# Performance work log

Measured on AMD Instinct MI355X. Metric: run time of the kernel, lower is better.

Reference implementation:

```python
import jax, jax.numpy as jnp
import numpy as np

B, N, DIM, H, DH, P = 4, 4096, 256, 8, 64, 2
INNER = H * DH  # 512


def setup_inputs() -> dict:
    key = jax.random.key(0)
    ks = jax.random.split(key, 10)
    w = lambda k, shape: jax.random.normal(k, shape, dtype=jnp.float32) * 0.02
    return dict(
        x=jax.random.normal(ks[0], (B, N, DIM), dtype=jnp.float32),
        prev_x=jax.random.normal(ks[1], (B, N, DIM), dtype=jnp.float32),
        ln_q_g=jnp.ones((2 * DIM,), jnp.float32), ln_q_b=jnp.zeros((2 * DIM,), jnp.float32),
        ln_k_g=jnp.ones((DIM,), jnp.float32), ln_k_b=jnp.zeros((DIM,), jnp.float32),
        ln_v_g=jnp.ones((DIM,), jnp.float32), ln_v_b=jnp.zeros((DIM,), jnp.float32),
        Wq=w(ks[2], (2 * DIM, INNER)),            # to_q, bias=False
        Wk=w(ks[3], (DIM, INNER)), bk=jnp.zeros((INNER,), jnp.float32),
        Wv=w(ks[4], (DIM, INNER)), bv=jnp.zeros((INNER,), jnp.float32),
        Woff=w(ks[5], (H * P, INNER)),            # 1x1 conv == linear over channels
        boff=jax.random.uniform(ks[6], (H * P,), jnp.float32, -1.0, 1.0),
        Wout=w(ks[7], (DIM, INNER)), bout=jnp.zeros((DIM,), jnp.float32),
    )


def _ln(x, g, b):
    m = x.mean(-1, keepdims=True)
    v = ((x - m) ** 2).mean(-1, keepdims=True)
    return (x - m) * jax.lax.rsqrt(v + 1e-5) * g + b


def reference(x, prev_x, ln_q_g, ln_q_b, ln_k_g, ln_k_b, ln_v_g, ln_v_b,
              Wq, Wk, bk, Wv, bv, Woff, boff, Wout, bout):
    scale = DH ** -0.5
    # queries from cat(x, prev_x) along feature dim
    q = _ln(jnp.concatenate([x, prev_x], axis=-1), ln_q_g, ln_q_b) @ Wq  # (B,N,INNER)
    # learned per-head, per-point offsets (1x1 conv over channels)
    offsets = (q @ Woff.T + boff).reshape(B, N, H, P).transpose(0, 2, 3, 1)  # (B,H,P,N)
    # K/V from cat(x, prev_x) along batch dim -> KV length 2N per (b,h)
    kv = jnp.concatenate([x, prev_x], axis=0)  # (2B,N,DIM)
    k = (_ln(kv, ln_k_g, ln_k_b) @ Wk + bk).reshape(2, B, N, H, DH).transpose(1, 3, 4, 0, 2).reshape(B, H, DH, 2 * N)
    v = (_ln(kv, ln_v_g, ln_v_b) @ Wv + bv).reshape(2, B, N, H, DH).transpose(1, 3, 4, 0, 2).reshape(B, H, DH, 2 * N)
    # sampling positions: pos + offset, clamped, truncated to int (matches torch .long())
    pos = jnp.arange(N, dtype=jnp.float32)
    samp = jnp.clip(pos[None, None, None, :] + offsets, 0, 2 * N - 1).astype(jnp.int32)  # (B,H,P,N)
    idx = samp.transpose(0, 1, 3, 2)[:, :, None, :, :]  # (B,H,1,N,P)
    k_s = jnp.take_along_axis(k[:, :, :, None, :], idx, axis=-1)  # (B,H,DH,N,P)
    v_s = jnp.take_along_axis(v[:, :, :, None, :], idx, axis=-1)  # (B,H,DH,N,P)
    qh = q.reshape(B, N, H, DH).transpose(0, 2, 1, 3) * scale     # (B,H,N,DH)
    sim = jnp.einsum('bhnd,bhdnp->bhnp', qh, k_s)                  # (B,H,N,P)
    attn = jax.nn.softmax(sim, axis=-1)
    out = jnp.einsum('bhnp,bhdnp->bhnd', attn, v_s)                # (B,H,N,DH)
    out = out.transpose(0, 2, 1, 3).reshape(B, N, INNER) @ Wout.T + bout  # (B,N,DIM)
    return out, offsets
```

## Files before the change

### kernel.cpp

```cpp
#include <hip/hip_runtime.h>
#include <hip/hip_bf16.h>
#include <math.h>

#define B_    4
#define N_    4096
#define DIM_  256
#define H_    8
#define DH_   64
#define P_    2
#define INNER_ 512
#define BN_   (B_ * N_)
#define KVR_  (2 * BN_)

typedef short v8s  __attribute__((ext_vector_type(8)));
typedef short v4s  __attribute__((ext_vector_type(4)));
typedef float v4f  __attribute__((ext_vector_type(4)));

__device__ __forceinline__ short f2b(float x) {
    __hip_bfloat16 h = __float2bfloat16(x);
    return *reinterpret_cast<short*>(&h);
}
__device__ __forceinline__ float b2f(short s) {
    __hip_bfloat16 h = *reinterpret_cast<__hip_bfloat16*>(&s);
    return __bfloat162float(h);
}

__device__ __forceinline__ void async16(const void* g, void* l) {
    __builtin_amdgcn_global_load_lds(
        (const __attribute__((address_space(1))) void*)g,
        (__attribute__((address_space(3))) void*)l, 16, 0, 0);
}

__device__ __forceinline__ void storeRow(float* p, float4 f0, float4 f1, float4 f2, float4 f3) {
    ((float4*)p)[0] = f0; ((float4*)p)[1] = f1; ((float4*)p)[2] = f2; ((float4*)p)[3] = f3;
}
__device__ __forceinline__ void storeRow(__hip_bfloat16* p, float4 f0, float4 f1, float4 f2, float4 f3) {
    v8s o0, o1;
    o0[0]=f2b(f0.x); o0[1]=f2b(f0.y); o0[2]=f2b(f0.z); o0[3]=f2b(f0.w);
    o0[4]=f2b(f1.x); o0[5]=f2b(f1.y); o0[6]=f2b(f1.z); o0[7]=f2b(f1.w);
    o1[0]=f2b(f2.x); o1[1]=f2b(f2.y); o1[2]=f2b(f2.z); o1[3]=f2b(f2.w);
    o1[4]=f2b(f3.x); o1[5]=f2b(f3.y); o1[6]=f2b(f3.z); o1[7]=f2b(f3.w);
    ((v8s*)p)[0] = o0; ((v8s*)p)[1] = o1;
}

__global__ __launch_bounds__(256) void prep_all(
    const float* __restrict__ Wq, const float* __restrict__ gq, const float* __restrict__ betaq,
    const float* __restrict__ Wk, const float* __restrict__ gk, const float* __restrict__ betak,
    const float* __restrict__ bk,
    const float* __restrict__ Wv, const float* __restrict__ gv, const float* __restrict__ betav,
    const float* __restrict__ bv,
    const float* __restrict__ Woff, const float* __restrict__ Wout,
    short* __restrict__ Wq2t, float* __restrict__ bq2,
    short* __restrict__ Wkvt, float* __restrict__ bkv,
    float* __restrict__ Wcomb, float* __restrict__ braw, short* __restrict__ Woutb) {
    __shared__ float sm[272];
    const int bid = blockIdx.x, t = threadIdx.x;

    if (bid < 1536) {
        const float *W, *g, *beta, *bias_in;
        short* Wt; float* b2; int K, n; float scale;
        if (bid < 512)       { W=Wq; g=gq; beta=betaq; bias_in=nullptr; Wt=Wq2t; b2=bq2; K=512; n=bid;        scale=0.125f; }
        else if (bid < 1024) { W=Wk; g=gk; beta=betak; bias_in=bk; Wt=Wkvt;           b2=bkv;       K=256; n=bid-512;  scale=1.f; }
        else                 { W=Wv; g=gv; beta=betav; bias_in=bv; Wt=Wkvt+512*256;   b2=bkv+512;   K=256; n=bid-1024; scale=1.f; }
        float partial = 0.f;
        for (int k = t; k < K; k += 256) {
            float w = W[k * 512 + n];
            Wt[(size_t)n * K + k] = f2b(scale * g[k] * w);
            partial += beta[k] * w;
        }
        sm[t] = partial;
        __syncthreads();
        for (int s = 128; s > 0; s >>= 1) {
            if (t < s) sm[t] += sm[t + s];
            __syncthreads();
        }
        if (t == 0) b2[n] = scale * ((bias_in ? bias_in[n] : 0.f) + sm[0]);
    } else if (bid < 2048) {
        const int k = bid - 1536;
        const int hp = t & 15, jg = t >> 4;
        float p = 0.f;
        for (int j = jg; j < INNER_; j += 16)
            p += Wq[k * INNER_ + j] * Woff[hp * INNER_ + j];
        sm[jg * 17 + hp] = p;
        __syncthreads();
        if (t < 16) {
            float s = 0.f;
            for (int i = 0; i < 16; i++) s += sm[i * 17 + t];
            Wcomb[k * 16 + t] = gq[k] * s;
            braw[k * 16 + t]  = betaq[k] * s;
        }
    } else {
        const int i0 = (bid - 2048) * 1024 + t * 4;
        float4 f = *(const float4*)(Wout + i0);
        v4s o;
        o[0] = f2b(f.x); o[1] = f2b(f.y); o[2] = f2b(f.z); o[3] = f2b(f.w);
        *(v4s*)(Woutb + i0) = o;
    }
}

__global__ void bcomb_sum(const float* __restrict__ braw, const float* __restrict__ boff,
                          float* __restrict__ bcomb) {
    __shared__ float sm[272];
    int t = threadIdx.x;
    int hp = t & 15, kg = t >> 4;
    float p = 0.f;
    for (int k = kg; k < 512; k += 16) p += braw[k * 16 + hp];
    sm[kg * 17 + hp] = p;
    __syncthreads();
    if (t < 16) {
        float s = 0.f;
        for (int i = 0; i < 16; i++) s += sm[i * 17 + t];
        bcomb[t] = s + boff[t];
    }
}

__global__ __launch_bounds__(256) void norm_fused_kernel(
    const float* __restrict__ x, const float* __restrict__ p,
    const float* __restrict__ Wcomb, const float* __restrict__ bcomb,
    short* __restrict__ Aq, short* __restrict__ Akv,
    float* __restrict__ out_off, int* __restrict__ idx) {
    const int lane = threadIdx.x & 63;
    const int wv   = threadIdx.x >> 6;
    const int m0   = (blockIdx.x * 4 + wv) * 4;
    const int k8   = lane * 8;

    float4 w[8][4];
#pragma unroll
    for (int i = 0; i < 8; i++) {
        const float4* wr = (const float4*)(Wcomb + (size_t)(k8 + i) * 16);
#pragma unroll
        for (int j = 0; j < 4; j++) w[i][j] = wr[j];
    }
    const float bc = bcomb[lane & 15];

    const float* srcb = (lane < 32) ? (x + k8) : (p + k8 - DIM_);

    float4 u0 = ((const float4*)(srcb + (size_t)m0 * DIM_))[0];
    float4 u1 = ((const float4*)(srcb + (size_t)m0 * DIM_))[1];

#pragma unroll
    for (int r = 0; r < 4; r++) {
        const int m = m0 + r;
        float4 n0, n1;
        if (r < 3) {
            n0 = ((const float4*)(srcb + (size_t)(m + 1) * DIM_))[0];
            n1 = ((const float4*)(srcb + (size_t)(m + 1) * DIM_))[1];
        }
        float uv[8] = { u0.x, u0.y, u0.z, u0.w, u1.x, u1.y, u1.z, u1.w };

        float s = 0.f, q2 = 0.f;
#pragma unroll
        for (int i = 0; i < 8; i++) { s += uv[i]; q2 += uv[i] * uv[i]; }
#pragma unroll
        for (int d = 1; d <= 16; d <<= 1) {
            s  += __shfl_xor(s, d);
            q2 += __shfl_xor(q2, d);
        }
        float mean_h = s * (1.f / 256.f);
        float var_h  = q2 * (1.f / 256.f) - mean_h * mean_h;
        float rstd_h = rsqrtf(var_h + 1e-5f);
        float sf  = s  + __shfl_xor(s, 32);
        float q2f = q2 + __shfl_xor(q2, 32);
        float mean_q = sf * (1.f / 512.f);
        float var_q  = q2f * (1.f / 512.f) - mean_q * mean_q;
        float rstd_q = rsqrtf(var_q + 1e-5f);

        v8s okv;
#pragma unroll
        for (int i = 0; i < 8; i++) okv[i] = f2b((uv[i] - mean_h) * rstd_h);
        short* akvdst = Akv + ((lane < 32) ? ((size_t)m * DIM_ + k8)
                                           : ((size_t)(BN_ + m) * DIM_ + k8 - DIM_));
        *(v8s*)akvdst = okv;

        float nv[8];
        v8s oq;
#pragma unroll
        for (int i = 0; i < 8; i++) { nv[i] = (uv[i] - mean_q) * rstd_q; oq[i] = f2b(nv[i]); }
        *(v8s*)(Aq + (size_t)m * INNER_ + k8) = oq;

        float acc[16];
#pragma unroll
        for (int h = 0; h < 16; h++) acc[h] = 0.f;
#pragma unroll
        for (int i = 0; i < 8; i++) {
            float nvi = nv[i];
            acc[0]  += nvi * w[i][0].x;  acc[1]  += nvi * w[i][0].y;
            acc[2]  += nvi * w[i][0].z;  acc[3]  += nvi * w[i][0].w;
            acc[4]  += nvi * w[i][1].x;  acc[5]  += nvi * w[i][1].y;
            acc[6]  += nvi * w[i][1].z;  acc[7]  += nvi * w[i][1].w;
            acc[8]  += nvi * w[i][2].x;  acc[9]  += nvi * w[i][2].y;
            acc[10] += nvi * w[i][2].z;  acc[11] += nvi * w[i][2].w;
            acc[12] += nvi * w[i][3].x;  acc[13] += nvi * w[i][3].y;
            acc[14] += nvi * w[i][3].z;  acc[15] += nvi * w[i][3].w;
        }
        float a8[8];
#pragma unroll
        for (int j = 0; j < 8; j++) {
            float lo = acc[2 * j] + __shfl_xor(acc[2 * j], 1);
            float hi = acc[2 * j + 1] + __shfl_xor(acc[2 * j + 1], 1);
            a8[j] = (lane & 1) ? hi : lo;
        }
        float a4[4];
#pragma unroll
        for (int j = 0; j < 4; j++) {
            float lo = a8[2 * j] + __shfl_xor(a8[2 * j], 2);
            float hi = a8[2 * j + 1] + __shfl_xor(a8[2 * j + 1], 2);
            a4[j] = (lane & 2) ? hi : lo;
        }
        float a2[2];
#pragma unroll
        for (int j = 0; j < 2; j++) {
            float lo = a4[2 * j] + __shfl_xor(a4[2 * j], 4);
            float hi = a4[2 * j + 1] + __shfl_xor(a4[2 * j + 1], 4);
            a2[j] = (lane & 4) ? hi : lo;
        }
        float l1 = a2[0] + __shfl_xor(a2[0], 8);
        float h1 = a2[1] + __shfl_xor(a2[1], 8);
        float a1 = (lane & 8) ? h1 : l1;
        a1 += __shfl_xor(a1, 16);
        a1 += __shfl_xor(a1, 32);

        if (lane < 16) {
            float off = a1 + bc;
            int b = m >> 12, n = m & (N_ - 1);
            int h = lane >> 1, pp = lane & 1;
            out_off[(size_t)((b * H_ + h) * P_ + pp) * N_ + n] = off;
            float f = fminf(fmaxf((float)n + off, 0.f), (float)(2 * N_ - 1));
            idx[((size_t)(b * H_ + h) * N_ + n) * P_ + pp] = (int)f;
        }
        u0 = n0; u1 = n1;
    }
}

template <typename OT>
__device__ __forceinline__ void gemm_body(
    short* smem, const short* __restrict__ A, const short* __restrict__ Bt,
    const float* __restrict__ bias, OT* __restrict__ C, int N, int K, int nx, int lin) {
    short* As = smem;
    short* Bs = smem + 128 * 64;
    const int tid  = threadIdx.x;
    const int lane = tid & 63, w = tid >> 6;
    const int wr = w >> 1, wc = w & 1;
    const int lm = lane & 15, g = lane >> 4;

    const int x8 = lin & 7, t = lin >> 3;
    const int bx = t % nx, by = (t / nx) * 8 + x8;
    const int row0 = by * 128, col0 = bx * 128;

    const short* pa[4];
    const short* pb[4];
#pragma unroll
    for (int r = 0; r < 4; r++) {
        int s   = tid + 256 * r;
        int row = s >> 3, kcs = s & 7;
        int kg  = kcs ^ (row & 7);
        pa[r] = A  + (size_t)(row0 + row) * K + kg * 8;
        pb[r] = Bt + (size_t)(col0 + row) * K + kg * 8;
    }

    v4f acc[4][4];
#pragma unroll
    for (int i = 0; i < 4; i++)
#pragma unroll
        for (int j = 0; j < 4; j++) acc[i][j] = (v4f){0.f, 0.f, 0.f, 0.f};

    for (int k0 = 0; k0 < K; k0 += 64) {
        __syncthreads();
#pragma unroll
        for (int r = 0; r < 4; r++) {
            int s = tid + 256 * r;
            async16(pa[r] + k0, (char*)As + s * 16);
            async16(pb[r] + k0, (char*)Bs + s * 16);
        }
        __syncthreads();
#pragma unroll
        for (int ks = 0; ks < 2; ks++) {
            v8s af[4], bf[4];
#pragma unroll
            for (int i = 0; i < 4; i++) {
                int m   = wr * 64 + i * 16 + lm;
                int sch = m * 8 + ((ks * 4 + g) ^ (m & 7));
                af[i] = *(const v8s*)(As + sch * 8);
            }
#pragma unroll
            for (int j = 0; j < 4; j++) {
                int n   = wc * 64 + j * 16 + lm;
                int sch = n * 8 + ((ks * 4 + g) ^ (n & 7));
                bf[j] = *(const v8s*)(Bs + sch * 8);
            }
#pragma unroll
            for (int i = 0; i < 4; i++)
#pragma unroll
                for (int j = 0; j < 4; j++)
                    acc[i][j] = __builtin_amdgcn_mfma_f32_16x16x32_bf16(af[i], bf[j], acc[i][j], 0, 0, 0);
        }
    }

#pragma unroll
    for (int j = 0; j < 4; j++) {
        int gc = col0 + wc * 64 + j * 16 + lm;
        float bj = bias ? bias[gc] : 0.f;
#pragma unroll
        for (int i = 0; i < 4; i++)
#pragma unroll
            for (int r = 0; r < 4; r++) acc[i][j][r] += bj;
    }

    __syncthreads();
    float* ep = (float*)smem + w * (16 * 68);
#pragma unroll
    for (int i = 0; i < 4; i++) {
#pragma unroll
        for (int j = 0; j < 4; j++)
#pragma unroll
            for (int r = 0; r < 4; r++)
                ep[(g * 4 + r) * 68 + j * 16 + lm] = acc[i][j][r];
        asm volatile("s_waitcnt lgkmcnt(0)" ::: "memory");
        int rr = lane >> 2, cb = (lane & 3) * 16;
        float4 f0 = *(float4*)(ep + rr * 68 + cb + 0);
        float4 f1 = *(float4*)(ep + rr * 68 + cb + 4);
        float4 f2 = *(float4*)(ep + rr * 68 + cb + 8);
        float4 f3 = *(float4*)(ep + rr * 68 + cb + 12);
        asm volatile("s_waitcnt lgkmcnt(0)" ::: "memory");
        int grow = row0 + wr * 64 + i * 16 + rr;
        int gcol = col0 + wc * 64 + cb;
        storeRow(&C[(size_t)grow * N + gcol], f0, f1, f2, f3);
    }
}

#define ATILE_ (256 * 64)

__global__ __launch_bounds__(512, 2) void gemm_qkv_256(
    const short* __restrict__ Aqp, const short* __restrict__ Wq2t,
    const float* __restrict__ bq2, __hip_bfloat16* __restrict__ qb,
    const short* __restrict__ Akvp, const short* __restrict__ Wkvt,
    const float* __restrict__ bkv, __hip_bfloat16* __restrict__ kvproj) {
    __shared__ short smem[4 * ATILE_];

    const short* A; const short* Bt; const float* bias; __hip_bfloat16* C;
    int N, K, NT, nxs, nwg, lin;
    if ((int)blockIdx.x < 128) {
        A = Aqp;  Bt = Wq2t; bias = bq2; C = qb;
        N = 512;  K = 512; NT = 8; nxs = 1; nwg = 128; lin = blockIdx.x;
    } else {
        A = Akvp; Bt = Wkvt; bias = bkv; C = kvproj;
        N = 1024; K = 256; NT = 4; nxs = 2; nwg = 512; lin = blockIdx.x - 128;
    }

    const int tid  = threadIdx.x;
    const int lane = tid & 63, w = tid >> 6;
    const int wr = w >> 2, wc = w & 3;
    const int lm = lane & 15, g = lane >> 4;

    const int wg = (lin & 7) * (nwg >> 3) + (lin >> 3);
    const int bx = wg & ((1 << nxs) - 1), by = wg >> nxs;
    const int row0 = by << 8, col0 = bx << 8;

    short* As0 = smem;
    short* Bs0 = smem + 2 * ATILE_;

    const int kg = ((tid & 7) ^ ((tid >> 3) & 7)) << 3;
    const short* gA = A  + (size_t)(row0 + (tid >> 3)) * K + kg;
    const short* gB = Bt + (size_t)(col0 + (tid >> 3)) * K + kg;

    auto stage = [&](int buf, int k0, int which) {
        const short* gp; char* lp;
        if (which < 2) { gp = gA + (size_t)which * 128 * K;
                         lp = (char*)(As0 + buf * ATILE_) + which * 16384; }
        else           { gp = gB + (size_t)(which - 2) * 128 * K;
                         lp = (char*)(Bs0 + buf * ATILE_) + (which - 2) * 16384; }
        async16(gp + k0,                  lp + tid * 16);
        async16(gp + k0 + (size_t)64 * K, lp + 8192 + tid * 16);
    };

    v4f acc[8][4];
#pragma unroll
    for (int i = 0; i < 8; i++)
#pragma unroll
        for (int j = 0; j < 4; j++) acc[i][j] = (v4f){0.f, 0.f, 0.f, 0.f};

    float bj[4];
#pragma unroll
    for (int jj = 0; jj < 4; jj++) bj[jj] = bias[col0 + wc * 64 + jj * 16 + lm];

    v8s aF[4][2];
    v8s bF0[2][2], bF1[2][2];

    auto RD_A = [&](const short* base, int qi) {
#pragma unroll
        for (int i = 0; i < 4; i++) {
            const int m = wr * 128 + qi * 64 + i * 16 + lm;
#pragma unroll
            for (int ks = 0; ks < 2; ks++)
                aF[i][ks] = *(const v8s*)(base + m * 64 + (((ks << 2) | g) ^ (m & 7)) * 8);
        }
    };
    auto RD_B = [&](const short* base, int qj, v8s (*bf)[2]) {
#pragma unroll
        for (int j = 0; j < 2; j++) {
            const int n = wc * 64 + qj * 32 + j * 16 + lm;
#pragma unroll
            for (int ks = 0; ks < 2; ks++)
                bf[j][ks] = *(const v8s*)(base + n * 64 + (((ks << 2) | g) ^ (n & 7)) * 8);
        }
    };
    auto MFMA_Q = [&](int qi, int qj, v8s (*bf)[2]) {
        __builtin_amdgcn_s_setprio(1);
#pragma unroll
        for (int i = 0; i < 4; i++)
#pragma unroll
            for (int j = 0; j < 2; j++) {
                acc[qi*4+i][qj*2+j] = __builtin_amdgcn_mfma_f32_16x16x32_bf16(aF[i][0], bf[j][0], acc[qi*4+i][qj*2+j], 0, 0, 0);
                acc[qi*4+i][qj*2+j] = __builtin_amdgcn_mfma_f32_16x16x32_bf16(aF[i][1], bf[j][1], acc[qi*4+i][qj*2+j], 0, 0, 0);
            }
        __builtin_amdgcn_s_setprio(0);
    };

    stage(0, 0, 2); stage(0, 0, 3); stage(0, 0, 0); stage(0, 0, 1);
    stage(1, 64, 2); stage(1, 64, 3);
    asm volatile("s_waitcnt vmcnt(4)" ::: "memory");
    __builtin_amdgcn_s_barrier();
    asm volatile("" ::: "memory");

    for (int T = 0; T < NT; ++T) {
        const int cur = T & 1;
        const short* as = As0 + cur * ATILE_;
        const short* bs = Bs0 + cur * ATILE_;
        const bool sA = (T + 1 < NT);
        const bool sB = (T + 2 < NT);
        const int kA = (T + 1) << 6, kB = (T + 2) << 6;

        RD_A(as, 0); RD_B(bs, 0, bF0);
        if (sA) stage(cur ^ 1, kA, 0);
        __builtin_amdgcn_s_barrier();
        asm volatile("s_waitcnt lgkmcnt(0)" ::: "memory");
        MFMA_Q(0, 0, bF0);
        __builtin_amdgcn_s_barrier();

        RD_B(bs, 1, bF1);
        if (sA) stage(cur ^ 1, kA, 1);
        __builtin_amdgcn_s_barrier();
        asm volatile("s_waitcnt lgkmcnt(0)" ::: "memory");
        MFMA_Q(0, 1, bF1);
        __builtin_amdgcn_s_barrier();

        RD_A(as, 1);
        if (sB) stage(cur, kB, 2);
        __builtin_amdgcn_s_barrier();
        asm volatile("s_waitcnt lgkmcnt(0)" ::: "memory");
        MFMA_Q(1, 1, bF1);
        __builtin_amdgcn_s_barrier();

        if (sB) stage(cur, kB, 3);
        __builtin_amdgcn_s_barrier();
        MFMA_Q(1, 0, bF0);
        if (sB)      asm volatile("s_waitcnt vmcnt(4)" ::: "memory");
        else if (sA) asm volatile("s_waitcnt vmcnt(0)" ::: "memory");
        __builtin_amdgcn_s_barrier();
        asm volatile("" ::: "memory");
    }

    float* ep = (float*)smem + w * (16 * 68);
#pragma unroll
    for (int ii = 0; ii < 8; ii++) {
#pragma unroll
        for (int jj = 0; jj < 4; jj++)
#pragma unroll
            for (int r = 0; r < 4; r++)
                ep[(g * 4 + r) * 68 + jj * 16 + lm] = acc[ii][jj][r] + bj[jj];
        asm volatile("s_waitcnt lgkmcnt(0)" ::: "memory");
        const int rr = lane >> 2, cb = (lane & 3) * 16;
        float4 f0 = *(float4*)(ep + rr * 68 + cb + 0);
        float4 f1 = *(float4*)(ep + rr * 68 + cb + 4);
        float4 f2 = *(float4*)(ep + rr * 68 + cb + 8);
        float4 f3 = *(float4*)(ep + rr * 68 + cb + 12);
        asm volatile("s_waitcnt lgkmcnt(0)" ::: "memory");
        const int grow = row0 + wr * 128 + ii * 16 + rr;
        const int gcol = col0 + wc * 64 + cb;
        storeRow(&C[(size_t)grow * N + gcol], f0, f1, f2, f3);
    }
}

__global__ __launch_bounds__(256) void gemm_out(
    const short* __restrict__ A, const short* __restrict__ Bt,
    const float* __restrict__ bias, float* __restrict__ C) {
    __shared__ short smem[2 * 128 * 64];
    const int lin = blockIdx.y * gridDim.x + blockIdx.x;
    gemm_body<float>(smem, A, Bt, bias, C, 256, 512, 2, lin);
}

__global__ __launch_bounds__(256) void attn_kernel(
    const short* __restrict__ qb, const short* __restrict__ kvproj,
    const int* __restrict__ idx, short* __restrict__ attnout) {
    const int lane = threadIdx.x & 63;
    const int wv   = threadIdx.x >> 6;
    const int s    = lane >> 4, c = lane & 15;
    const int n = blockIdx.x * 16 + wv * 4 + s;
    const int h = blockIdx.y, b = blockIdx.z;
    const int m = b * N_ + n;

    v4s qv = *(const v4s*)(qb + (size_t)m * INNER_ + h * DH_ + c * 4);

    const int* ip = idx + ((size_t)(b * H_ + h) * N_ + n) * P_;
    int j0 = ip[0], j1 = ip[1];
    int r0 = b * N_ + j0 + ((j0 >= N_) ? (BN_ - N_) : 0);
    int r1 = b * N_ + j1 + ((j1 >= N_) ? (BN_ - N_) : 0);
    const short* k0p = kvproj + (size_t)r0 * 1024 + h * DH_ + c * 4;
    const short* k1p = kvproj + (size_t)r1 * 1024 + h * DH_ + c * 4;
    v4s k0 = *(const v4s*)k0p, v0 = *(const v4s*)(k0p + 512);
    v4s k1 = *(const v4s*)k1p, v1 = *(const v4s*)(k1p + 512);

    float q0 = b2f(qv[0]), q1 = b2f(qv[1]), q2 = b2f(qv[2]), q3 = b2f(qv[3]);
    float s0 = q0 * b2f(k0[0]) + q1 * b2f(k0[1]) + q2 * b2f(k0[2]) + q3 * b2f(k0[3]);
    float s1 = q0 * b2f(k1[0]) + q1 * b2f(k1[1]) + q2 * b2f(k1[2]) + q3 * b2f(k1[3]);
#pragma unroll
    for (int d = 1; d <= 8; d <<= 1) {
        s0 += __shfl_xor(s0, d);
        s1 += __shfl_xor(s1, d);
    }
    float mx = fmaxf(s0, s1);
    float e0 = __expf(s0 - mx), e1 = __expf(s1 - mx);
    float inv = 1.f / (e0 + e1);
    v4s o;
#pragma unroll
    for (int i = 0; i < 4; i++)
        o[i] = f2b((e0 * b2f(v0[i]) + e1 * b2f(v1[i])) * inv);
    *(v4s*)(attnout + (size_t)m * INNER_ + h * DH_ + c * 4) = o;
}

extern "C" void kernel_launch(void* const* d_in, const int* in_sizes, int n_in,
                              void* d_out, int out_size, void* d_ws, size_t ws_size,
                              hipStream_t stream) {
    (void)in_sizes; (void)n_in; (void)out_size; (void)ws_size;

    const float* x      = (const float*)d_in[0];
    const float* prevx  = (const float*)d_in[1];
    const float* ln_q_g = (const float*)d_in[2];
    const float* ln_q_b = (const float*)d_in[3];
    const float* ln_k_g = (const float*)d_in[4];
    const float* ln_k_b = (const float*)d_in[5];
    const float* ln_v_g = (const float*)d_in[6];
    const float* ln_v_b = (const float*)d_in[7];
    const float* Wq     = (const float*)d_in[8];
    const float* Wk     = (const float*)d_in[9];
    const float* bk     = (const float*)d_in[10];
    const float* Wv     = (const float*)d_in[11];
    const float* bv     = (const float*)d_in[12];
    const float* Woff   = (const float*)d_in[13];
    const float* boff   = (const float*)d_in[14];
    const float* Wout   = (const float*)d_in[15];
    const float* bout   = (const float*)d_in[16];

    char* cur = (char*)d_ws;
    auto alloc = [&](size_t bytes) { char* p = cur; cur += (bytes + 255) & ~(size_t)255; return p; };
    short* Aq      = (short*)alloc((size_t)BN_ * INNER_ * 2);
    short* Akv     = (short*)alloc((size_t)KVR_ * DIM_ * 2);
    short* qb      = (short*)alloc((size_t)BN_ * INNER_ * 2);
    short* kvproj  = (short*)alloc((size_t)KVR_ * 1024 * 2);
    short* attnout = (short*)alloc((size_t)BN_ * INNER_ * 2);
    short* Wq2t    = (short*)alloc(512 * 512 * 2);
    short* Wkvt    = (short*)alloc(1024 * 256 * 2);
    short* Woutb   = (short*)alloc(256 * 512 * 2);
    float* bq2     = (float*)alloc(512 * 4);
    float* bkv     = (float*)alloc(1024 * 4);
    float* Wcomb   = (float*)alloc(512 * 16 * 4);
    float* braw    = (float*)alloc(512 * 16 * 4);
    float* bcomb   = (float*)alloc(16 * 4);
    int*   idxb    = (int*)alloc((size_t)BN_ * 16 * 4);

    float* out_main = (float*)d_out;
    float* out_off  = out_main + (size_t)BN_ * DIM_;

    prep_all<<<2176, 256, 0, stream>>>(Wq, ln_q_g, ln_q_b,
                                       Wk, ln_k_g, ln_k_b, bk,
                                       Wv, ln_v_g, ln_v_b, bv,
                                       Woff, Wout,
                                       Wq2t, bq2, Wkvt, bkv, Wcomb, braw, Woutb);
    bcomb_sum<<<1, 256, 0, stream>>>(braw, boff, bcomb);

    norm_fused_kernel<<<BN_ / 16, 256, 0, stream>>>(x, prevx, Wcomb, bcomb,
                                                    Aq, Akv, out_off, idxb);

    gemm_qkv_256<<<640, 512, 0, stream>>>(Aq, Wq2t, bq2, (__hip_bfloat16*)qb,
                                          Akv, Wkvt, bkv, (__hip_bfloat16*)kvproj);

    dim3 ga(N_ / 16, H_, B_);
    attn_kernel<<<ga, 256, 0, stream>>>(qb, kvproj, idxb, attnout);

    gemm_out<<<dim3(2, 128), 256, 0, stream>>>(attnout, Woutb, bout, out_main);
}
```

Measured before the change: 218.1 us.

## Restructure GEMM main loop into two half-phases with deeper A/B prefetch

Replaces the four-quadrant schedule with two half-tile phases: all B fragments plus half of A are read, then the next-next B tile is staged, and similarly for A. Prefetch distance for A grows from one to two tiles, with vmcnt waits adjusted to 8 outstanding loads, and there are fewer barriers per iteration. The aim is to cut synchronization overhead and hide global load latency better. The cost is more fragment registers (full B plus two A halves live at once), which may reduce occupancy or cause spills.

```diff
diff --git a/kernel.cpp b/kernel.cpp
--- a/kernel.cpp
+++ b/kernel.cpp
@@ -363,15 +363,18 @@
     const short* gA = A  + (size_t)(row0 + (tid >> 3)) * K + kg;
     const short* gB = Bt + (size_t)(col0 + (tid >> 3)) * K + kg;
 
-    auto stage = [&](int buf, int k0, int which) {
-        const short* gp; char* lp;
-        if (which < 2) { gp = gA + (size_t)which * 128 * K;
-                         lp = (char*)(As0 + buf * ATILE_) + which * 16384; }
-        else           { gp = gB + (size_t)(which - 2) * 128 * K;
-                         lp = (char*)(Bs0 + buf * ATILE_) + (which - 2) * 16384; }
-        async16(gp + k0,                  lp + tid * 16);
-        async16(gp + k0 + (size_t)64 * K, lp + 8192 + tid * 16);
+    auto stageA = [&](int buf, int k0) {
+        char* lp = (char*)(As0 + buf * ATILE_);
+#pragma unroll
+        for (int r = 0; r < 4; r++)
+            async16(gA + (size_t)r * 64 * K + k0, lp + r * 8192 + tid * 16);
     };
+    auto stageB = [&](int buf, int k0) {
+        char* lp = (char*)(Bs0 + buf * ATILE_);
+#pragma unroll
+        for (int r = 0; r < 4; r++)
+            async16(gB + (size_t)r * 64 * K + k0, lp + r * 8192 + tid * 16);
+    };
 
     v4f acc[8][4];
 #pragma unroll
@@ -383,42 +386,41 @@
 #pragma unroll
     for (int jj = 0; jj < 4; jj++) bj[jj] = bias[col0 + wc * 64 + jj * 16 + lm];
 
-    v8s aF[4][2];
-    v8s bF0[2][2], bF1[2][2];
-
-    auto RD_A = [&](const short* base, int qi) {
+    v8s aLo[4][2], aHi[4][2], bF[4][2];
+
+    auto RD_A = [&](const short* base, int half, v8s (*dst)[2]) {
 #pragma unroll
         for (int i = 0; i < 4; i++) {
-            const int m = wr * 128 + qi * 64 + i * 16 + lm;
+            const int m = wr * 128 + half * 64 + i * 16 + lm;
 #pragma unroll
             for (int ks = 0; ks < 2; ks++)
-                aF[i][ks] = *(const v8s*)(base + m * 64 + (((ks << 2) | g) ^ (m & 7)) * 8);
+                dst[i][ks] = *(const v8s*)(base + m * 64 + (((ks << 2) | g) ^ (m & 7)) * 8);
         }
     };
-    auto RD_B = [&](const short* base, int qj, v8s (*bf)[2]) {
-#pragma unroll
-        for (int j = 0; j < 2; j++) {
-            const int n = wc * 64 + qj * 32 + j * 16 + lm;
+    auto RD_B = [&](const short* base) {
+#pragma unroll
+        for (int j = 0; j < 4; j++) {
+            const int n = wc * 64 + j * 16 + lm;
 #pragma unroll
             for (int ks = 0; ks < 2; ks++)
-                bf[j][ks] = *(const v8s*)(base + n * 64 + (((ks << 2) | g) ^ (n & 7)) * 8);
+                bF[j][ks] = *(const v8s*)(base + n * 64 + (((ks << 2) | g) ^ (n & 7)) * 8);
         }
     };
-    auto MFMA_Q = [&](int qi, int qj, v8s (*bf)[2]) {
+    auto MFMA_H = [&](int half, v8s (*af)[2]) {
         __builtin_amdgcn_s_setprio(1);
 #pragma unroll
         for (int i = 0; i < 4; i++)
 #pragma unroll
-            for (int j = 0; j < 2; j++) {
-                acc[qi*4+i][qj*2+j] = __builtin_amdgcn_mfma_f32_16x16x32_bf16(aF[i][0], bf[j][0], acc[qi*4+i][qj*2+j], 0, 0, 0);
-                acc[qi*4+i][qj*2+j] = __builtin_amdgcn_mfma_f32_16x16x32_bf16(aF[i][1], bf[j][1], acc[qi*4+i][qj*2+j], 0, 0, 0);
+            for (int j = 0; j < 4; j++) {
+                acc[half*4+i][j] = __builtin_amdgcn_mfma_f32_16x16x32_bf16(af[i][0], bF[j][0], acc[half*4+i][j], 0, 0, 0);
+                acc[half*4+i][j] = __builtin_amdgcn_mfma_f32_16x16x32_bf16(af[i][1], bF[j][1], acc[half*4+i][j], 0, 0, 0);
             }
         __builtin_amdgcn_s_setprio(0);
     };
 
-    stage(0, 0, 2); stage(0, 0, 3); stage(0, 0, 0); stage(0, 0, 1);
-    stage(1, 64, 2); stage(1, 64, 3);
-    asm volatile("s_waitcnt vmcnt(4)" ::: "memory");
+    stageB(0, 0); stageA(0, 0);
+    stageB(1, 64); stageA(1, 64);
+    asm volatile("s_waitcnt vmcnt(8)" ::: "memory");
     __builtin_amdgcn_s_barrier();
     asm volatile("" ::: "memory");
 
@@ -426,36 +428,22 @@
         const int cur = T & 1;
         const short* as = As0 + cur * ATILE_;
         const short* bs = Bs0 + cur * ATILE_;
-        const bool sA = (T + 1 < NT);
-        const bool sB = (T + 2 < NT);
-        const int kA = (T + 1) << 6, kB = (T + 2) << 6;
-
-        RD_A(as, 0); RD_B(bs, 0, bF0);
-        if (sA) stage(cur ^ 1, kA, 0);
+        const bool s2 = (T + 2 < NT);
+        const int k2 = (T + 2) << 6;
+
+        RD_B(bs);
+        RD_A(as, 0, aLo);
+        asm volatile("s_waitcnt lgkmcnt(0)" ::: "memory");
         __builtin_amdgcn_s_barrier();
+        if (s2) stageB(cur, k2);
+        MFMA_H(0, aLo);
+        RD_A(as, 1, aHi);
         asm volatile("s_waitcnt lgkmcnt(0)" ::: "memory");
-        MFMA_Q(0, 0, bF0);
         __builtin_amdgcn_s_barrier();
-
-        RD_B(bs, 1, bF1);
-        if (sA) stage(cur ^ 1, kA, 1);
-        __builtin_amdgcn_s_barrier();
-        asm volatile("s_waitcnt lgkmcnt(0)" ::: "memory");
-        MFMA_Q(0, 1, bF1);
-        __builtin_amdgcn_s_barrier();
-
-        RD_A(as, 1);
-        if (sB) stage(cur, kB, 2);
-        __builtin_amdgcn_s_barrier();
-        asm volatile("s_waitcnt lgkmcnt(0)" ::: "memory");
-        MFMA_Q(1, 1, bF1);
-        __builtin_amdgcn_s_barrier();
-
-        if (sB) stage(cur, kB, 3);
-        __builtin_amdgcn_s_barrier();
-        MFMA_Q(1, 0, bF0);
-        if (sB)      asm volatile("s_waitcnt vmcnt(4)" ::: "memory");
-        else if (sA) asm volatile("s_waitcnt vmcnt(0)" ::: "memory");
+        if (s2) stageA(cur, k2);
+        MFMA_H(1, aHi);
+        if (s2)              asm volatile("s_waitcnt vmcnt(8)" ::: "memory");
+        else if (T + 1 < NT) asm volatile("s_waitcnt vmcnt(0)" ::: "memory");
         __builtin_amdgcn_s_barrier();
         asm volatile("" ::: "memory");
     }
```

After: 216.4 us. Within noise of the previous version (-0.8%).
